# Kernel optimization log

Hardware: AMD Instinct MI355X
Metric: run time of the kernel (lower is better)

Reference implementation:

```python
import jax, jax.numpy as jnp
import numpy as np

N, G, H = 500_000, 25_000, 256


def setup_inputs() -> dict:
    key = jax.random.key(0)
    ks = jax.random.split(key, 8)
    node = jax.random.normal(ks[0], (N, H), dtype=jnp.float32)
    super_node = jax.random.normal(ks[1], (G, H), dtype=jnp.float32)
    segment_ids = jnp.sort(jax.random.randint(ks[2], (N,), 0, G, dtype=jnp.int32))
    s = 0.05
    return {
        "node": node,
        "super_node": super_node,
        "segment_ids": segment_ids,
        "w_align": jax.random.normal(ks[3], (2 * H, 1), jnp.float32) * s,
        "b_align": jnp.zeros((1,), jnp.float32),
        "w_attend": jax.random.normal(ks[4], (H, H), jnp.float32) * s,
        "b_attend": jnp.zeros((H,), jnp.float32),
        "w_ih": jax.random.normal(ks[5], (H, 3 * H), jnp.float32) * s,
        "w_hh": jax.random.normal(ks[6], (H, 3 * H), jnp.float32) * s,
        "b_ih": jnp.zeros((3 * H,), jnp.float32),
        "b_hh": jnp.zeros((3 * H,), jnp.float32),
    }


def reference(node, super_node, segment_ids, w_align, b_align, w_attend,
              b_attend, w_ih, w_hh, b_ih, b_hh):
    g = super_node.shape[0]
    h = node.shape[1]
    # super_node = F.leaky_relu(super_node)
    s = jax.nn.leaky_relu(super_node)  # slope 0.01 (torch default)
    # cal_alignment(cat([node, broadcast_nodes(super)])) == node@Wn + (s@Ws)[seg]
    wn, ws = w_align[:h], w_align[h:]
    score = jax.nn.leaky_relu(node @ wn + (s @ ws)[segment_ids] + b_align)  # [N,1]
    # softmax_nodes: segment-wise stable softmax
    m = jax.ops.segment_max(score, segment_ids, num_segments=g)
    w = jnp.exp(score - m[segment_ids])
    denom = jax.ops.segment_sum(w, segment_ids, num_segments=g)
    attn = w / denom[segment_ids]  # [N,1]
    # attend (dropout=0, eval)
    hidden = node @ w_attend + b_attend  # [N,H]
    # sum_nodes weighted by attention, then ELU
    ctx = jax.nn.elu(jax.ops.segment_sum(attn * hidden, segment_ids, num_segments=g))  # [G,H]
    # GRUCell(ctx, s) per torch semantics
    gi = ctx @ w_ih + b_ih
    gh = s @ w_hh + b_hh
    ir, iz, inn = jnp.split(gi, 3, axis=-1)
    hr, hz, hn = jnp.split(gh, 3, axis=-1)
    r = jax.nn.sigmoid(ir + hr)
    z = jax.nn.sigmoid(iz + hz)
    n = jnp.tanh(inn + r * hn)
    new_h = (1.0 - z) * n + z * s
    return jax.nn.relu(new_h), attn
```

## Files before the change

### kernel.cpp

```cpp
#include <hip/hip_runtime.h>
#include <math.h>

#define N_NODES 500000
#define G_SEG   25000
#define H_DIM   256
#define SPB     4

typedef __attribute__((ext_vector_type(4))) float f32x4;
typedef __attribute__((ext_vector_type(8))) short bf16x8;

__device__ __forceinline__ float leaky(float x){ return x > 0.f ? x : 0.01f * x; }

__device__ __forceinline__ ushort f2bf(float f){
  unsigned u = __float_as_uint(f);
  u += 0x7FFFu + ((u >> 16) & 1u);
  return (ushort)(u >> 16);
}

__global__ __launch_bounds__(256) void k_starts(
    const int* __restrict__ seg, int* __restrict__ starts)
{
  int i = blockIdx.x * 256 + threadIdx.x;
  if (i >= N_NODES) return;
  int s = seg[i];
  int prev = (i == 0) ? -1 : seg[i - 1];
  for (int g = prev + 1; g <= s; g++) starts[g] = i;
  if (i == N_NODES - 1)
    for (int g = s + 1; g <= G_SEG; g++) starts[g] = N_NODES;
}

__global__ __launch_bounds__(256) void k0_prep_w(
    const float* __restrict__ w_att, ushort* __restrict__ Bp)
{
  int kk = blockIdx.x, n = threadIdx.x;
  Bp[(((kk >> 3) << 8) + n) * 8 + (kk & 7)] = f2bf(w_att[kk * H_DIM + n]);
}

__global__ __launch_bounds__(256) void k0b_prep_w6(
    const float* __restrict__ w_ih, const float* __restrict__ w_hh,
    ushort* __restrict__ Bp6)
{
  int kk = blockIdx.x;
  int c  = threadIdx.x;
  #pragma unroll
  for (int gate = 0; gate < 4; gate++) {
    float v;
    if (gate == 0)      v = (kk < 256) ? w_ih[kk * 768 + c]        : w_hh[(kk - 256) * 768 + c];
    else if (gate == 1) v = (kk < 256) ? w_ih[kk * 768 + 256 + c]  : w_hh[(kk - 256) * 768 + 256 + c];
    else if (gate == 2) v = (kk < 256) ? w_ih[kk * 768 + 512 + c]  : 0.f;
    else                v = (kk < 256) ? 0.f                       : w_hh[(kk - 256) * 768 + 512 + c];
    int n = (gate << 8) + c;
    Bp6[(((kk >> 3) << 10) + n) * 8 + (kk & 7)] = f2bf(v);
  }
}

__global__ __launch_bounds__(256) void k1_prep_super(
    const float* __restrict__ sn, const float* __restrict__ w_align,
    float* __restrict__ s_buf, float* __restrict__ sws)
{
  int g = blockIdx.x, t = threadIdx.x;
  float v = sn[g * H_DIM + t];
  float sv = leaky(v);
  s_buf[g * H_DIM + t] = sv;
  float p = sv * w_align[H_DIM + t];
  #pragma unroll
  for (int d = 1; d < 64; d <<= 1) p += __shfl_xor(p, d);
  __shared__ float red[4];
  int wid = t >> 6, lane = t & 63;
  if (lane == 0) red[wid] = p;
  __syncthreads();
  if (t == 0) sws[g] = red[0] + red[1] + red[2] + red[3];
}

__global__ __launch_bounds__(256) void kF_score_softmax_agg(
    const float* __restrict__ node, const int* __restrict__ starts,
    const float* __restrict__ w_align, const float* __restrict__ b_align,
    const float* __restrict__ sws, float* __restrict__ score,
    float* __restrict__ attn_out, float* __restrict__ agg,
    float* __restrict__ bscale)
{
  __shared__ float cpart[4][H_DIM];
  __shared__ float wm[4], wsum[4];
  __shared__ int st_s[SPB + 1];

  const int tid = threadIdx.x;
  const int g0 = blockIdx.x * SPB;
  if (tid <= SPB) st_s[tid] = starts[g0 + tid];
  __syncthreads();

  const int wv = tid >> 6, lane = tid & 63;
  const float4 wvec = ((const float4*)w_align)[lane];
  const float b0 = b_align[0];

  for (int j = 0; j < SPB; j++) {
    const int g = g0 + j;
    const int st = st_s[j], en = st_s[j + 1];
    const float swsg = sws[g];

    float m = -3.4e38f, sum = 0.f;
    f32x4 pacc = {0.f, 0.f, 0.f, 0.f};

    for (int r = st + wv; r < en; r += 4) {
      f32x4 a = ((const f32x4*)node)[(size_t)r * 64 + lane];
      float d = a[0] * wvec.x + a[1] * wvec.y + a[2] * wvec.z + a[3] * wvec.w;
      #pragma unroll
      for (int m2 = 1; m2 < 64; m2 <<= 1) d += __shfl_xor(d, m2);
      float sc = leaky(d + swsg + b0);
      if (lane == 0) score[r] = sc;
      if (sc <= m) {
        float p = __expf(sc - m);
        sum += p;
        pacc += p * a;
      } else {
        float scale = __expf(m - sc);
        sum = sum * scale + 1.f;
        pacc = pacc * scale + a;
        m = sc;
      }
    }

    if (j > 0) __syncthreads();
    ((f32x4*)&cpart[wv][0])[lane] = pacc;
    if (lane == 0) { wm[wv] = m; wsum[wv] = sum; }
    __syncthreads();

    float m0 = fmaxf(fmaxf(wm[0], wm[1]), fmaxf(wm[2], wm[3]));
    float f0 = (wm[0] > -1e38f) ? __expf(wm[0] - m0) : 0.f;
    float f1 = (wm[1] > -1e38f) ? __expf(wm[1] - m0) : 0.f;
    float f2 = (wm[2] > -1e38f) ? __expf(wm[2] - m0) : 0.f;
    float f3 = (wm[3] > -1e38f) ? __expf(wm[3] - m0) : 0.f;
    float D = wsum[0] * f0 + wsum[1] * f1 + wsum[2] * f2 + wsum[3] * f3;
    float invD = (D > 0.f) ? 1.f / D : 0.f;

    float v = cpart[0][tid] * f0 + cpart[1][tid] * f1 +
              cpart[2][tid] * f2 + cpart[3][tid] * f3;
    agg[(size_t)g * H_DIM + tid] = v * invD;
    if (tid == 0) bscale[g] = (D > 0.f) ? 1.f : 0.f;

    for (int r = st + tid; r < en; r += 256)
      attn_out[r] = __expf(score[r] - m0) * invD;
  }
}

__global__ __launch_bounds__(256, 2) void k5b_ctx(
    const float* __restrict__ agg, const ushort* __restrict__ Bp,
    const float* __restrict__ b_att, const float* __restrict__ bscale,
    float* __restrict__ ctx)
{
  __shared__ __align__(16) ushort A_lds[128 * 256];

  const int tid  = threadIdx.x;
  const int row0 = blockIdx.x * 128;

  #pragma unroll
  for (int i = 0; i < 16; i++) {
    int v = tid + i * 256;
    int r = v >> 5;
    int s = v & 31;
    int grow = row0 + r;
    f32x4 x0 = {0.f, 0.f, 0.f, 0.f}, x1 = {0.f, 0.f, 0.f, 0.f};
    if (grow < G_SEG) {
      const f32x4* p = (const f32x4*)(agg + (size_t)grow * H_DIM) + s * 2;
      x0 = p[0]; x1 = p[1];
    }
    bf16x8 t;
    t[0] = (short)f2bf(x0[0]); t[1] = (short)f2bf(x0[1]);
    t[2] = (short)f2bf(x0[2]); t[3] = (short)f2bf(x0[3]);
    t[4] = (short)f2bf(x1[0]); t[5] = (short)f2bf(x1[1]);
    t[6] = (short)f2bf(x1[2]); t[7] = (short)f2bf(x1[3]);
    *(bf16x8*)&A_lds[r * 256 + ((s ^ (r & 7)) * 8)] = t;
  }
  __syncthreads();

  const int wv  = tid >> 6;
  const int l   = tid & 63;
  const int l15 = l & 15, lq = l >> 4, l7 = l & 7;
  const int colbase = wv * 64 + l15;

  f32x4 acc[8][4];
  #pragma unroll
  for (int mf = 0; mf < 8; mf++)
    #pragma unroll
    for (int nf = 0; nf < 4; nf++)
      acc[mf][nf] = (f32x4){0.f, 0.f, 0.f, 0.f};

  for (int ks = 0; ks < 8; ks++) {
    int c = ks * 4 + lq;
    bf16x8 b[4];
    #pragma unroll
    for (int nf = 0; nf < 4; nf++)
      b[nf] = *(const bf16x8*)&Bp[(((c << 8) + colbase + nf * 16)) * 8];
    bf16x8 a[8];
    #pragma unroll
    for (int mf = 0; mf < 8; mf++)
      a[mf] = *(const bf16x8*)&A_lds[(mf * 16 + l15) * 256 + ((c ^ l7) * 8)];
    #pragma unroll
    for (int mf = 0; mf < 8; mf++)
      #pragma unroll
      for (int nf = 0; nf < 4; nf++)
        acc[mf][nf] = __builtin_amdgcn_mfma_f32_16x16x32_bf16(
            a[mf], b[nf], acc[mf][nf], 0, 0, 0);
  }

  float bias[4];
  #pragma unroll
  for (int nf = 0; nf < 4; nf++) bias[nf] = b_att[colbase + nf * 16];

  #pragma unroll
  for (int mf = 0; mf < 8; mf++) {
    #pragma unroll
    for (int r = 0; r < 4; r++) {
      int grow = row0 + mf * 16 + lq * 4 + r;
      if (grow < G_SEG) {
        float bsc = bscale[grow];
        #pragma unroll
        for (int nf = 0; nf < 4; nf++)
          ctx[(size_t)grow * H_DIM + colbase + nf * 16] =
              acc[mf][nf][r] + bias[nf] * bsc;
      }
    }
  }
}

__global__ __launch_bounds__(256, 2) void k6_mfma(
    const float* __restrict__ ctxbuf, const float* __restrict__ s_buf,
    const ushort* __restrict__ Bp6,
    const float* __restrict__ b_ih, const float* __restrict__ b_hh,
    float* __restrict__ out0)
{
  __shared__ __align__(16) ushort A_lds[32 * 512];

  const int tid  = threadIdx.x;
  const int row0 = blockIdx.x * 32;

  #pragma unroll
  for (int i = 0; i < 8; i++) {
    int v = tid + i * 256;
    int r = v >> 6;
    int s = v & 63;
    int g = row0 + r;
    f32x4 x0 = {0.f, 0.f, 0.f, 0.f}, x1 = {0.f, 0.f, 0.f, 0.f};
    if (g < G_SEG) {
      const f32x4* p = (s < 32)
          ? (const f32x4*)(ctxbuf + (size_t)g * H_DIM) + s * 2
          : (const f32x4*)(s_buf + (size_t)g * H_DIM) + (s - 32) * 2;
      x0 = p[0]; x1 = p[1];
      if (s < 32) {
        #pragma unroll
        for (int e = 0; e < 4; e++) {
          x0[e] = x0[e] > 0.f ? x0[e] : (__expf(x0[e]) - 1.f);
          x1[e] = x1[e] > 0.f ? x1[e] : (__expf(x1[e]) - 1.f);
        }
      }
    }
    bf16x8 t;
    t[0] = (short)f2bf(x0[0]); t[1] = (short)f2bf(x0[1]);
    t[2] = (short)f2bf(x0[2]); t[3] = (short)f2bf(x0[3]);
    t[4] = (short)f2bf(x1[0]); t[5] = (short)f2bf(x1[1]);
    t[6] = (short)f2bf(x1[2]); t[7] = (short)f2bf(x1[3]);
    *(bf16x8*)&A_lds[r * 512 + ((s ^ (r & 7)) * 8)] = t;
  }
  __syncthreads();

  const int wv  = tid >> 6;
  const int l   = tid & 63;
  const int l15 = l & 15, lq = l >> 4, l7 = l & 7;

  f32x4 acc[4][2][4];
  #pragma unroll
  for (int gt = 0; gt < 4; gt++)
    #pragma unroll
    for (int mf = 0; mf < 2; mf++)
      #pragma unroll
      for (int nf = 0; nf < 4; nf++)
        acc[gt][mf][nf] = (f32x4){0.f, 0.f, 0.f, 0.f};

  for (int ks = 0; ks < 16; ks++) {
    int c = ks * 4 + lq;
    bf16x8 a[2];
    #pragma unroll
    for (int mf = 0; mf < 2; mf++)
      a[mf] = *(const bf16x8*)&A_lds[(mf * 16 + l15) * 512 + ((c ^ l7) * 8)];
    #pragma unroll
    for (int gt = 0; gt < 4; gt++) {
      if (gt == 2 && ks >= 8) continue;
      if (gt == 3 && ks < 8) continue;
      #pragma unroll
      for (int nf = 0; nf < 4; nf++) {
        int n = (gt << 8) + (wv << 6) + nf * 16 + l15;
        bf16x8 b = *(const bf16x8*)&Bp6[(((c << 10) + n)) * 8];
        acc[gt][0][nf] = __builtin_amdgcn_mfma_f32_16x16x32_bf16(
            a[0], b, acc[gt][0][nf], 0, 0, 0);
        acc[gt][1][nf] = __builtin_amdgcn_mfma_f32_16x16x32_bf16(
            a[1], b, acc[gt][1][nf], 0, 0, 0);
      }
    }
  }

  #pragma unroll
  for (int nf = 0; nf < 4; nf++) {
    int cc = (wv << 6) + nf * 16 + l15;
    float bir = b_ih[cc] + b_hh[cc];
    float biz = b_ih[256 + cc] + b_hh[256 + cc];
    float bin_ = b_ih[512 + cc];
    float bhn  = b_hh[512 + cc];
    #pragma unroll
    for (int mf = 0; mf < 2; mf++) {
      #pragma unroll
      for (int rr = 0; rr < 4; rr++) {
        int grow = row0 + mf * 16 + lq * 4 + rr;
        if (grow < G_SEG) {
          float v0 = acc[0][mf][nf][rr];
          float v1 = acc[1][mf][nf][rr];
          float v2 = acc[2][mf][nf][rr];
          float v3 = acc[3][mf][nf][rr];
          float r_ = 1.f / (1.f + __expf(-(v0 + bir)));
          float z_ = 1.f / (1.f + __expf(-(v1 + biz)));
          float n_ = tanhf(v2 + bin_ + r_ * (v3 + bhn));
          float sv = s_buf[(size_t)grow * H_DIM + cc];
          float nh = (1.f - z_) * n_ + z_ * sv;
          out0[(size_t)grow * H_DIM + cc] = nh > 0.f ? nh : 0.f;
        }
      }
    }
  }
}

extern "C" void kernel_launch(void* const* d_in, const int* in_sizes, int n_in,
                              void* d_out, int out_size, void* d_ws, size_t ws_size,
                              hipStream_t stream)
{
  (void)in_sizes; (void)n_in; (void)out_size; (void)ws_size;
  const float* node       = (const float*)d_in[0];
  const float* super_node = (const float*)d_in[1];
  const int*   seg        = (const int*)d_in[2];
  const float* w_align    = (const float*)d_in[3];
  const float* b_align    = (const float*)d_in[4];
  const float* w_att      = (const float*)d_in[5];
  const float* b_att      = (const float*)d_in[6];
  const float* w_ih       = (const float*)d_in[7];
  const float* w_hh       = (const float*)d_in[8];
  const float* b_ih       = (const float*)d_in[9];
  const float* b_hh       = (const float*)d_in[10];

  float* out0     = (float*)d_out;
  float* attn_out = (float*)d_out + (size_t)G_SEG * H_DIM;

  float* ws     = (float*)d_ws;
  float* s_buf  = ws;
  float* score  = ws + 6400000;
  float* sws    = ws + 6900000;
  float* ctx    = ws + 6925000;
  float* agg    = ws + 13325000;
  ushort* Bp    = (ushort*)(ws + 19725000);
  ushort* Bp6   = (ushort*)(ws + 19760000);
  float* bscale = ws + 20025000;
  int*   starts = (int*)(ws + 20050000);

  k_starts<<<(N_NODES + 255) / 256, 256, 0, stream>>>(seg, starts);
  k0_prep_w<<<H_DIM, H_DIM, 0, stream>>>(w_att, Bp);
  k0b_prep_w6<<<512, 256, 0, stream>>>(w_ih, w_hh, Bp6);
  k1_prep_super<<<G_SEG, 256, 0, stream>>>(super_node, w_align, s_buf, sws);
  kF_score_softmax_agg<<<G_SEG / SPB, 256, 0, stream>>>(
      node, starts, w_align, b_align, sws, score, attn_out, agg, bscale);
  k5b_ctx<<<(G_SEG + 127) / 128, 256, 0, stream>>>(agg, Bp, b_att, bscale, ctx);
  k6_mfma<<<(G_SEG + 31) / 32, 256, 0, stream>>>(ctx, s_buf, Bp6, b_ih, b_hh, out0);
}
```

Before: 289.1 us.

## Unroll node streaming loop 4x, reuse attn output as score scratch, merge pack kernels

The main score/softmax/aggregate loop now processes four node rows per wave per iteration. This issues four independent 1 KB loads and interleaves their shuffle reductions to raise memory-level parallelism and hide latency, and the online-softmax max update is done once per batch of four. Scores are written straight into the attention output buffer and rescaled in place, which drops the separate score workspace. The two weight-pack kernels are merged into one launch. The cost is more registers per thread and a scalar tail loop for leftover rows.

```diff
diff --git a/kernel.cpp b/kernel.cpp
--- a/kernel.cpp
+++ b/kernel.cpp
@@ -29,28 +29,27 @@
     for (int g = s + 1; g <= G_SEG; g++) starts[g] = N_NODES;
 }
 
-__global__ __launch_bounds__(256) void k0_prep_w(
-    const float* __restrict__ w_att, ushort* __restrict__ Bp)
-{
-  int kk = blockIdx.x, n = threadIdx.x;
-  Bp[(((kk >> 3) << 8) + n) * 8 + (kk & 7)] = f2bf(w_att[kk * H_DIM + n]);
-}
-
-__global__ __launch_bounds__(256) void k0b_prep_w6(
-    const float* __restrict__ w_ih, const float* __restrict__ w_hh,
+__global__ __launch_bounds__(256) void kPack(
+    const float* __restrict__ w_att, const float* __restrict__ w_ih,
+    const float* __restrict__ w_hh, ushort* __restrict__ Bp,
     ushort* __restrict__ Bp6)
 {
-  int kk = blockIdx.x;
-  int c  = threadIdx.x;
-  #pragma unroll
-  for (int gate = 0; gate < 4; gate++) {
-    float v;
-    if (gate == 0)      v = (kk < 256) ? w_ih[kk * 768 + c]        : w_hh[(kk - 256) * 768 + c];
-    else if (gate == 1) v = (kk < 256) ? w_ih[kk * 768 + 256 + c]  : w_hh[(kk - 256) * 768 + 256 + c];
-    else if (gate == 2) v = (kk < 256) ? w_ih[kk * 768 + 512 + c]  : 0.f;
-    else                v = (kk < 256) ? 0.f                       : w_hh[(kk - 256) * 768 + 512 + c];
-    int n = (gate << 8) + c;
-    Bp6[(((kk >> 3) << 10) + n) * 8 + (kk & 7)] = f2bf(v);
+  int b = blockIdx.x, c = threadIdx.x;
+  if (b < 256) {
+    int kk = b;
+    Bp[(((kk >> 3) << 8) + c) * 8 + (kk & 7)] = f2bf(w_att[kk * H_DIM + c]);
+  } else {
+    int kk = b - 256;
+    #pragma unroll
+    for (int gate = 0; gate < 4; gate++) {
+      float v;
+      if (gate == 0)      v = (kk < 256) ? w_ih[kk * 768 + c]        : w_hh[(kk - 256) * 768 + c];
+      else if (gate == 1) v = (kk < 256) ? w_ih[kk * 768 + 256 + c]  : w_hh[(kk - 256) * 768 + 256 + c];
+      else if (gate == 2) v = (kk < 256) ? w_ih[kk * 768 + 512 + c]  : 0.f;
+      else                v = (kk < 256) ? 0.f                       : w_hh[(kk - 256) * 768 + 512 + c];
+      int n = (gate << 8) + c;
+      Bp6[(((kk >> 3) << 10) + n) * 8 + (kk & 7)] = f2bf(v);
+    }
   }
 }
 
@@ -75,7 +74,7 @@
 __global__ __launch_bounds__(256) void kF_score_softmax_agg(
     const float* __restrict__ node, const int* __restrict__ starts,
     const float* __restrict__ w_align, const float* __restrict__ b_align,
-    const float* __restrict__ sws, float* __restrict__ score,
+    const float* __restrict__ sws,
     float* __restrict__ attn_out, float* __restrict__ agg,
     float* __restrict__ bscale)
 {
@@ -100,13 +99,49 @@
     float m = -3.4e38f, sum = 0.f;
     f32x4 pacc = {0.f, 0.f, 0.f, 0.f};
 
-    for (int r = st + wv; r < en; r += 4) {
+    int r = st + wv;
+    for (; r + 12 < en; r += 16) {
+      f32x4 a0 = ((const f32x4*)node)[(size_t)(r     ) * 64 + lane];
+      f32x4 a1 = ((const f32x4*)node)[(size_t)(r +  4) * 64 + lane];
+      f32x4 a2 = ((const f32x4*)node)[(size_t)(r +  8) * 64 + lane];
+      f32x4 a3 = ((const f32x4*)node)[(size_t)(r + 12) * 64 + lane];
+      float d0 = a0[0]*wvec.x + a0[1]*wvec.y + a0[2]*wvec.z + a0[3]*wvec.w;
+      float d1 = a1[0]*wvec.x + a1[1]*wvec.y + a1[2]*wvec.z + a1[3]*wvec.w;
+      float d2 = a2[0]*wvec.x + a2[1]*wvec.y + a2[2]*wvec.z + a2[3]*wvec.w;
+      float d3 = a3[0]*wvec.x + a3[1]*wvec.y + a3[2]*wvec.z + a3[3]*wvec.w;
+      #pragma unroll
+      for (int s2 = 1; s2 < 64; s2 <<= 1) {
+        d0 += __shfl_xor(d0, s2);
+        d1 += __shfl_xor(d1, s2);
+        d2 += __shfl_xor(d2, s2);
+        d3 += __shfl_xor(d3, s2);
+      }
+      float sc0 = leaky(d0 + swsg + b0);
+      float sc1 = leaky(d1 + swsg + b0);
+      float sc2 = leaky(d2 + swsg + b0);
+      float sc3 = leaky(d3 + swsg + b0);
+      if (lane == 0) {
+        attn_out[r] = sc0; attn_out[r + 4] = sc1;
+        attn_out[r + 8] = sc2; attn_out[r + 12] = sc3;
+      }
+      float bm = fmaxf(fmaxf(sc0, sc1), fmaxf(sc2, sc3));
+      if (bm > m) {
+        float scale = __expf(m - bm);
+        sum *= scale; pacc *= scale; m = bm;
+      }
+      float p0 = __expf(sc0 - m), p1 = __expf(sc1 - m);
+      float p2 = __expf(sc2 - m), p3 = __expf(sc3 - m);
+      sum += (p0 + p1) + (p2 + p3);
+      pacc += p0 * a0 + p1 * a1;
+      pacc += p2 * a2 + p3 * a3;
+    }
+    for (; r < en; r += 4) {
       f32x4 a = ((const f32x4*)node)[(size_t)r * 64 + lane];
-      float d = a[0] * wvec.x + a[1] * wvec.y + a[2] * wvec.z + a[3] * wvec.w;
-      #pragma unroll
-      for (int m2 = 1; m2 < 64; m2 <<= 1) d += __shfl_xor(d, m2);
+      float d = a[0]*wvec.x + a[1]*wvec.y + a[2]*wvec.z + a[3]*wvec.w;
+      #pragma unroll
+      for (int s2 = 1; s2 < 64; s2 <<= 1) d += __shfl_xor(d, s2);
       float sc = leaky(d + swsg + b0);
-      if (lane == 0) score[r] = sc;
+      if (lane == 0) attn_out[r] = sc;
       if (sc <= m) {
         float p = __expf(sc - m);
         sum += p;
@@ -137,8 +172,8 @@
     agg[(size_t)g * H_DIM + tid] = v * invD;
     if (tid == 0) bscale[g] = (D > 0.f) ? 1.f : 0.f;
 
-    for (int r = st + tid; r < en; r += 256)
-      attn_out[r] = __expf(score[r] - m0) * invD;
+    for (int rr = st + tid; rr < en; rr += 256)
+      attn_out[rr] = __expf(attn_out[rr] - m0) * invD;
   }
 }
 
@@ -348,21 +383,19 @@
 
   float* ws     = (float*)d_ws;
   float* s_buf  = ws;
-  float* score  = ws + 6400000;
-  float* sws    = ws + 6900000;
-  float* ctx    = ws + 6925000;
-  float* agg    = ws + 13325000;
-  ushort* Bp    = (ushort*)(ws + 19725000);
-  ushort* Bp6   = (ushort*)(ws + 19760000);
-  float* bscale = ws + 20025000;
-  int*   starts = (int*)(ws + 20050000);
+  float* sws    = ws + 6400000;
+  float* agg    = ws + 6425000;
+  ushort* Bp    = (ushort*)(ws + 12825000);
+  ushort* Bp6   = (ushort*)(ws + 12860000);
+  float* bscale = ws + 13125000;
+  int*   starts = (int*)(ws + 13150000);
+  float* ctx    = ws + 13200000;
 
   k_starts<<<(N_NODES + 255) / 256, 256, 0, stream>>>(seg, starts);
-  k0_prep_w<<<H_DIM, H_DIM, 0, stream>>>(w_att, Bp);
-  k0b_prep_w6<<<512, 256, 0, stream>>>(w_ih, w_hh, Bp6);
+  kPack<<<768, 256, 0, stream>>>(w_att, w_ih, w_hh, Bp, Bp6);
   k1_prep_super<<<G_SEG, 256, 0, stream>>>(super_node, w_align, s_buf, sws);
   kF_score_softmax_agg<<<G_SEG / SPB, 256, 0, stream>>>(
-      node, starts, w_align, b_align, sws, score, attn_out, agg, bscale);
+      node, starts, w_align, b_align, sws, attn_out, agg, bscale);
   k5b_ctx<<<(G_SEG + 127) / 128, 256, 0, stream>>>(agg, Bp, b_att, bscale, ctx);
   k6_mfma<<<(G_SEG + 31) / 32, 256, 0, stream>>>(ctx, s_buf, Bp6, b_ih, b_hh, out0);
 }
```

Measured after the change: 277.6 us. 1.04x faster.
